# Kernel tuning notes

Measured on AMD Instinct MI355X. Metric: run time of the kernel, lower is better.

Reference implementation:

```python
import jax, jax.numpy as jnp
import numpy as np

B, N, D = 4096, 32768, 256


def setup_inputs() -> dict:
    key = jax.random.key(0)
    kx, kp = jax.random.split(key)
    x = jax.random.normal(kx, (B, D), dtype=jnp.float32)
    prototypes = jax.random.normal(kp, (N, D), dtype=jnp.float32)
    return {"x": x, "prototypes": prototypes}


def reference(x, prototypes):
    # Brute-force L2 1-NN: faiss IndexFlatL2 exact search, k=1, then gather
    x_sq = jnp.sum(x * x, axis=-1, keepdims=True)            # [B, 1]
    p_sq = jnp.sum(prototypes * prototypes, axis=-1)          # [N]
    dists = x_sq + p_sq[None, :] - 2.0 * (x @ prototypes.T)   # [B, N]
    idx = jnp.argmin(dists, axis=-1)                          # [B]
    return prototypes[idx]                                    # [B, D]
```

## Files before the change

### kernel.cpp

```cpp
#include <hip/hip_runtime.h>
#include <stdint.h>


#define NB 4096
#define NP 32768
#define ND 256
#define NG 512
#define MARGIN 2.0f
#define NSPLIT 8
#define CPB 4096

typedef __attribute__((ext_vector_type(8))) __bf16 bf16x8;
typedef __attribute__((ext_vector_type(4))) __bf16 bf16x4;
typedef __attribute__((ext_vector_type(4))) float f32x4;

static constexpr size_t OFF_PSQ = 0;
static constexpr size_t OFF_XB  = 131072;
static constexpr size_t OFF_PB  = OFF_XB + (size_t)NB * ND * 2;
static constexpr size_t OFF_BM  = OFF_PB + (size_t)NP * ND * 2;
static constexpr size_t WS_NEED = OFF_BM + (size_t)NB * NG * 4;

#define VMCNT(n) asm volatile("s_waitcnt vmcnt(" #n ")" ::: "memory")

__device__ __forceinline__ void gload_lds16(const void* g, void* l) {
    __builtin_amdgcn_global_load_lds(
        (const __attribute__((address_space(1))) uint32_t*)g,
        (__attribute__((address_space(3))) uint32_t*)l, 16, 0, 0);
}
__device__ __forceinline__ unsigned fkey(float f) {
    unsigned u = __float_as_uint(f);
    return (u & 0x80000000u) ? ~u : (u | 0x80000000u);
}
__device__ __forceinline__ float fkey_inv(unsigned u) {
    unsigned o = (u & 0x80000000u) ? (u & 0x7FFFFFFFu) : ~u;
    return __uint_as_float(o);
}
__device__ __forceinline__ unsigned long long umin64(unsigned long long a,
                                                     unsigned long long b) {
    return a < b ? a : b;
}
__device__ __forceinline__ unsigned umin32(unsigned a, unsigned b) {
    return a < b ? a : b;
}

__global__ void prep_kernel(const float* __restrict__ X, const float* __restrict__ P,
                            float* __restrict__ psq, __bf16* __restrict__ Xb,
                            __bf16* __restrict__ Pb) {
    int row  = blockIdx.x * 4 + (threadIdx.x >> 6);
    int lane = threadIdx.x & 63;
    if (row < NP) {
        f32x4 v = ((const f32x4*)(P + (size_t)row * ND))[lane];
        bf16x4 b;
        b.x = (__bf16)v.x; b.y = (__bf16)v.y; b.z = (__bf16)v.z; b.w = (__bf16)v.w;
        ((bf16x4*)(Pb + (size_t)row * ND))[lane] = b;
        float s = v.x*v.x + v.y*v.y + v.z*v.z + v.w*v.w;
        #pragma unroll
        for (int off = 32; off > 0; off >>= 1) s += __shfl_down(s, off);
        if (lane == 0) psq[row] = s;
    } else {
        int r = row - NP;
        f32x4 v = ((const f32x4*)(X + (size_t)r * ND))[lane];
        bf16x4 b;
        b.x = (__bf16)v.x; b.y = (__bf16)v.y; b.z = (__bf16)v.z; b.w = (__bf16)v.w;
        ((bf16x4*)(Xb + (size_t)r * ND))[lane] = b;
    }
}

__global__ __launch_bounds__(512, 2)
void nn_sweep8_kernel(const __bf16* __restrict__ Xb, const __bf16* __restrict__ Pb,
                      const float* __restrict__ psq,
                      unsigned* __restrict__ blockmin) {
    __shared__ __align__(16) char smem[114688];
    char*     ring    = smem;
    float*    psq_lds = (float*)(smem + 65536);
    unsigned* tbl     = (unsigned*)(smem + 81920);

    const int tid  = threadIdx.x;
    const int lane = tid & 63;
    const int wave = tid >> 6;
    const int wm = wave >> 2, wn = wave & 3;
    const int bid    = blockIdx.x;
    const int nsplit = bid & 7;
    const int mblk   = bid >> 3;
    const int bm     = mblk * 128;
    const int Nb     = nsplit * CPB;
    const int fr = lane & 15, kg = lane >> 4;
    const int wbase16 = (tid & ~63) * 16;

    bf16x8 a[4][8];
    #pragma unroll
    for (int mi = 0; mi < 4; ++mi)
        #pragma unroll
        for (int qq = 0; qq < 8; ++qq)
            a[mi][qq] = *(const bf16x8*)(Xb +
                (size_t)(bm + wm * 64 + mi * 16 + fr) * ND + qq * 32 + kg * 8);

    f32x4 acc[4][4];
    #pragma unroll
    for (int i = 0; i < 4; ++i)
        #pragma unroll
        for (int j = 0; j < 4; ++j) acc[i][j] = (f32x4){0.f, 0.f, 0.f, 0.f};

    auto stage = [&](int nn, int qq) {
        char* dst = ring + (size_t)(qq & 3) * 16384;
        const int colb = Nb + nn * 256;
        #pragma unroll
        for (int i = 0; i < 2; ++i) {
            const int c = i * 512 + tid;
            const int fn = c >> 6;
            const int l  = c & 63;
            gload_lds16(Pb + (size_t)(colb + fn * 16 + (l & 15)) * ND +
                            qq * 32 + (l >> 4) * 8,
                        dst + i * 8192 + wbase16);
        }
    };

    gload_lds16((const char*)(psq + Nb) + (size_t)tid * 16,
                (char*)psq_lds + wbase16);
    gload_lds16((const char*)(psq + Nb) + 8192 + (size_t)tid * 16,
                (char*)psq_lds + 8192 + wbase16);
    stage(0, 0); stage(0, 1); stage(0, 2);

    #pragma unroll 1
    for (int n = 0; n < 16; ++n) {
        #pragma unroll
        for (int q = 0; q < 8; ++q) {
            if (q == 6) { if (n == 15) { VMCNT(2); } else { VMCNT(4); } }
            else if (q == 7) { if (n == 15) { VMCNT(0); } else { VMCNT(4); } }
            else { VMCNT(4); }
            __builtin_amdgcn_s_barrier();
            __builtin_amdgcn_sched_barrier(0);

            if (q < 5) {
                stage(n, q + 3);
            } else if (n < 15) {
                stage(n + 1, q - 5);
            }

            const char* pc = ring + (size_t)(q & 3) * 16384;
            bf16x8 b[4];
            #pragma unroll
            for (int ni = 0; ni < 4; ++ni)
                b[ni] = *(const bf16x8*)(pc +
                         (size_t)((wn * 4 + ni) * 64 + lane) * 16);
            __builtin_amdgcn_s_setprio(1);
            #pragma unroll
            for (int mi = 0; mi < 4; ++mi)
                #pragma unroll
                for (int ni = 0; ni < 4; ++ni)
                    acc[mi][ni] = __builtin_amdgcn_mfma_f32_16x16x32_bf16(
                        a[mi][q], b[ni], acc[mi][ni], 0, 0, 0);
            __builtin_amdgcn_s_setprio(0);

            if (q == 7) {
                float cq[4];
                #pragma unroll
                for (int ni = 0; ni < 4; ++ni)
                    cq[ni] = psq_lds[n * 256 + wn * 64 + ni * 16 + fr];
                #pragma unroll
                for (int mi = 0; mi < 4; ++mi) {
                    #pragma unroll
                    for (int r = 0; r < 4; ++r) {
                        float d = fmaf(-2.f, acc[mi][0][r], cq[0]);
                        #pragma unroll
                        for (int ni = 1; ni < 4; ++ni)
                            d = fminf(d, fmaf(-2.f, acc[mi][ni][r], cq[ni]));
                        #pragma unroll
                        for (int m = 1; m < 16; m <<= 1)
                            d = fminf(d, __shfl_xor(d, m));
                        if (fr == 0)
                            tbl[(wm * 64 + mi * 16 + kg * 4 + r) * 64 +
                                (n * 4 + wn)] = fkey(d);
                    }
                }
                #pragma unroll
                for (int i = 0; i < 4; ++i)
                    #pragma unroll
                    for (int j = 0; j < 4; ++j)
                        acc[i][j] = (f32x4){0.f, 0.f, 0.f, 0.f};
            }
        }
    }

    __syncthreads();
    const int rl = tid >> 2;
    const int gb = (tid & 3) * 16;
    #pragma unroll
    for (int j = 0; j < 4; ++j) {
        *(uint4*)&blockmin[(size_t)(bm + rl) * NG + nsplit * 64 + gb + j * 4] =
            *(const uint4*)&tbl[rl * 64 + gb + j * 4];
    }
}

__global__ __launch_bounds__(256)
void rescore_kernel(const float* __restrict__ X, const float* __restrict__ P,
                    const float* __restrict__ psq,
                    const unsigned* __restrict__ blockmin,
                    float* __restrict__ out) {
    __shared__ float Xs[256];
    __shared__ float part[256];
    __shared__ unsigned keymin[256];
    __shared__ unsigned short cand[NG];
    __shared__ int cnt;
    __shared__ unsigned bcol_s;

    const int row = blockIdx.x;
    const int tid = threadIdx.x;
    const unsigned* bmr = blockmin + (size_t)row * NG;

    unsigned k0 = bmr[tid], k1 = bmr[tid + 256];
    if (tid < 64)
        ((f32x4*)Xs)[tid] = ((const f32x4*)(X + (size_t)row * ND))[tid];
    if (tid == 0) cnt = 0;
    keymin[tid] = umin32(k0, k1);
    __syncthreads();
    #pragma unroll
    for (int s = 128; s > 0; s >>= 1) {
        if (tid < s) keymin[tid] = umin32(keymin[tid], keymin[tid + s]);
        __syncthreads();
    }
    unsigned thr = fkey(fkey_inv(keymin[0]) + MARGIN);
    if (k0 <= thr) cand[atomicAdd(&cnt, 1)] = (unsigned short)tid;
    if (k1 <= thr) cand[atomicAdd(&cnt, 1)] = (unsigned short)(tid + 256);
    __syncthreads();

    const int n     = cnt;
    const int ct    = tid & 63;
    const int cpart = tid >> 6;
    unsigned long long best = 0xFFFFFFFFFFFFFFFFull;
    for (int c = 0; c < n; ++c) {
        int g = cand[c];
        int col = g * 64 + ct;
        const f32x4* p4 = (const f32x4*)(P + (size_t)col * ND + cpart * 64);
        const f32x4* x4 = (const f32x4*)(Xs + cpart * 64);
        float s = 0.f;
        #pragma unroll
        for (int i = 0; i < 16; ++i) {
            f32x4 pv = p4[i], xv = x4[i];
            s = fmaf(xv.x, pv.x, s); s = fmaf(xv.y, pv.y, s);
            s = fmaf(xv.z, pv.z, s); s = fmaf(xv.w, pv.w, s);
        }
        part[tid] = s;
        __syncthreads();
        if (tid < 64) {
            int col2 = g * 64 + tid;
            float tot = part[tid] + part[tid + 64] + part[tid + 128] + part[tid + 192];
            float d = fmaf(-2.f, tot, psq[col2]);
            best = umin64(best, ((unsigned long long)fkey(d) << 32) |
                                (unsigned long long)col2);
        }
        __syncthreads();
    }
    if (tid < 64) {
        #pragma unroll
        for (int m = 1; m < 64; m <<= 1)
            best = umin64(best, __shfl_xor(best, m));
        if (tid == 0) bcol_s = (unsigned)(best & 0xFFFFFFFFull);
    }
    __syncthreads();
    unsigned bc = bcol_s;
    if (tid < 64)
        ((f32x4*)(out + (size_t)row * ND))[tid] =
            ((const f32x4*)(P + (size_t)bc * ND))[tid];
}

#define BM1 128
#define BN1 128
#define BK1 32
#define LDA1 132

__global__ void psq_init_kernel(const float* __restrict__ P, float* __restrict__ psq,
                                unsigned long long* __restrict__ minpack) {
    int row  = blockIdx.x * 4 + (threadIdx.x >> 6);
    int lane = threadIdx.x & 63;
    float4 p4 = ((const float4*)(P + (size_t)row * ND))[lane];
    float s = p4.x*p4.x + p4.y*p4.y + p4.z*p4.z + p4.w*p4.w;
    #pragma unroll
    for (int off = 32; off > 0; off >>= 1) s += __shfl_down(s, off);
    if (lane == 0) psq[row] = s;
    int gid = blockIdx.x * blockDim.x + threadIdx.x;
    if (gid < NB) minpack[gid] = 0xFFFFFFFFFFFFFFFFull;
}

__global__ __launch_bounds__(256, 2)
void nn_main_kernel(const float* __restrict__ X, const float* __restrict__ P,
                    const float* __restrict__ psq,
                    unsigned long long* __restrict__ minpack) {
    __shared__ __align__(16) char smem_raw[2 * BK1 * LDA1 * 4];
    float (*As)[LDA1] = (float (*)[LDA1])smem_raw;
    float (*Bs)[LDA1] = (float (*)[LDA1])(smem_raw + BK1 * LDA1 * 4);
    const int bm  = blockIdx.y * BM1;
    const int bn  = blockIdx.x * BN1;
    const int tid = threadIdx.x;
    const int tx  = tid & 15;
    const int ty  = tid >> 4;
    float acc[8][8];
    #pragma unroll
    for (int i = 0; i < 8; ++i)
        #pragma unroll
        for (int j = 0; j < 8; ++j) acc[i][j] = 0.f;
    const int lrow = tid >> 3;
    const int lk   = (tid & 7) * 4;
    for (int k0 = 0; k0 < ND; k0 += BK1) {
        #pragma unroll
        for (int p = 0; p < 4; ++p) {
            int r = p * 32 + lrow;
            float4 a = *(const float4*)(X + (size_t)(bm + r) * ND + k0 + lk);
            As[lk+0][r] = a.x; As[lk+1][r] = a.y; As[lk+2][r] = a.z; As[lk+3][r] = a.w;
            float4 b = *(const float4*)(P + (size_t)(bn + r) * ND + k0 + lk);
            Bs[lk+0][r] = b.x; Bs[lk+1][r] = b.y; Bs[lk+2][r] = b.z; Bs[lk+3][r] = b.w;
        }
        __syncthreads();
        #pragma unroll 4
        for (int k = 0; k < BK1; ++k) {
            float4 a0 = *(const float4*)&As[k][ty*8];
            float4 a1 = *(const float4*)&As[k][ty*8 + 4];
            float4 b0 = *(const float4*)&Bs[k][tx*4];
            float4 b1 = *(const float4*)&Bs[k][64 + tx*4];
            float av[8] = {a0.x,a0.y,a0.z,a0.w,a1.x,a1.y,a1.z,a1.w};
            float bv[8] = {b0.x,b0.y,b0.z,b0.w,b1.x,b1.y,b1.z,b1.w};
            #pragma unroll
            for (int i = 0; i < 8; ++i)
                #pragma unroll
                for (int j = 0; j < 8; ++j)
                    acc[i][j] = fmaf(av[i], bv[j], acc[i][j]);
        }
        __syncthreads();
    }
    unsigned long long (*red)[16] = (unsigned long long (*)[16])smem_raw;
    float cj[8];
    int   jglob[8];
    #pragma unroll
    for (int j = 0; j < 8; ++j) {
        int c = (j < 4) ? (tx*4 + j) : (64 + tx*4 + (j - 4));
        jglob[j] = bn + c;
        cj[j]    = psq[bn + c];
    }
    #pragma unroll
    for (int i = 0; i < 8; ++i) {
        float best = 0.f; unsigned bidx = 0u; bool first = true;
        #pragma unroll
        for (int j = 0; j < 8; ++j) {
            float s = fmaf(-2.f, acc[i][j], cj[j]);
            if (first || s < best) { best = s; bidx = (unsigned)jglob[j]; first = false; }
        }
        unsigned u = fkey(best);
        red[ty*8 + i][tx] = ((unsigned long long)u << 32) | (unsigned long long)bidx;
    }
    __syncthreads();
    if (tid < BM1) {
        unsigned long long m = red[tid][0];
        #pragma unroll
        for (int t = 1; t < 16; ++t) m = umin64(m, red[tid][t]);
        atomicMin(&minpack[bm + tid], m);
    }
}

__global__ void gather_kernel(const float* __restrict__ P,
                              const unsigned long long* __restrict__ minpack,
                              float* __restrict__ out) {
    int row = blockIdx.x;
    unsigned idx = (unsigned)(minpack[row] & 0xFFFFFFFFull);
    int lane = threadIdx.x;
    ((float4*)(out + (size_t)row * ND))[lane] =
        ((const float4*)(P + (size_t)idx * ND))[lane];
}

extern "C" void kernel_launch(void* const* d_in, const int* in_sizes, int n_in,
                              void* d_out, int out_size, void* d_ws, size_t ws_size,
                              hipStream_t stream) {
    const float* X = (const float*)d_in[0];
    const float* P = (const float*)d_in[1];
    float* out = (float*)d_out;
    char* w = (char*)d_ws;

    if (ws_size >= WS_NEED) {
        float* psq = (float*)(w + OFF_PSQ);
        __bf16* Xb = (__bf16*)(w + OFF_XB);
        __bf16* Pb = (__bf16*)(w + OFF_PB);
        unsigned* blockmin = (unsigned*)(w + OFF_BM);

        prep_kernel<<<(NP + NB) / 4, 256, 0, stream>>>(X, P, psq, Xb, Pb);
        nn_sweep8_kernel<<<(NB / 128) * NSPLIT, 512, 0, stream>>>(Xb, Pb, psq,
                                                                  blockmin);
        rescore_kernel<<<NB, 256, 0, stream>>>(X, P, psq, blockmin, out);
    } else {
        float* psq = (float*)w;
        unsigned long long* minpack = (unsigned long long*)(w + (size_t)NP * 4);
        psq_init_kernel<<<NP / 4, 256, 0, stream>>>(P, psq, minpack);
        dim3 grid(NP / BN1, NB / BM1);
        nn_main_kernel<<<grid, dim3(256), 0, stream>>>(X, P, psq, minpack);
        gather_kernel<<<NB, 64, 0, stream>>>(P, minpack, out);
    }
}
```

Before: 193.5 us.

## Replace LDS-staged sweep with per-wave register-streamed prototype loads

```diff
diff --git a/kernel.cpp b/kernel.cpp
--- a/kernel.cpp
+++ b/kernel.cpp
@@ -7,8 +7,6 @@
 #define ND 256
 #define NG 512
 #define MARGIN 2.0f
-#define NSPLIT 8
-#define CPB 4096
 
 typedef __attribute__((ext_vector_type(8))) __bf16 bf16x8;
 typedef __attribute__((ext_vector_type(4))) __bf16 bf16x4;
@@ -20,13 +18,6 @@
 static constexpr size_t OFF_BM  = OFF_PB + (size_t)NP * ND * 2;
 static constexpr size_t WS_NEED = OFF_BM + (size_t)NB * NG * 4;
 
-#define VMCNT(n) asm volatile("s_waitcnt vmcnt(" #n ")" ::: "memory")
-
-__device__ __forceinline__ void gload_lds16(const void* g, void* l) {
-    __builtin_amdgcn_global_load_lds(
-        (const __attribute__((address_space(1))) uint32_t*)g,
-        (__attribute__((address_space(3))) uint32_t*)l, 16, 0, 0);
-}
 __device__ __forceinline__ unsigned fkey(float f) {
     unsigned u = __float_as_uint(f);
     return (u & 0x80000000u) ? ~u : (u | 0x80000000u);
@@ -66,34 +57,27 @@
     }
 }
 
-__global__ __launch_bounds__(512, 2)
-void nn_sweep8_kernel(const __bf16* __restrict__ Xb, const __bf16* __restrict__ Pb,
+__global__ __launch_bounds__(256, 2)
+void nn_stream_kernel(const __bf16* __restrict__ Xb, const __bf16* __restrict__ Pb,
                       const float* __restrict__ psq,
                       unsigned* __restrict__ blockmin) {
-    __shared__ __align__(16) char smem[114688];
-    char*     ring    = smem;
-    float*    psq_lds = (float*)(smem + 65536);
-    unsigned* tbl     = (unsigned*)(smem + 81920);
-
     const int tid  = threadIdx.x;
     const int lane = tid & 63;
     const int wave = tid >> 6;
-    const int wm = wave >> 2, wn = wave & 3;
     const int bid    = blockIdx.x;
-    const int nsplit = bid & 7;
-    const int mblk   = bid >> 3;
-    const int bm     = mblk * 128;
-    const int Nb     = nsplit * CPB;
+    const int rowblk = bid >> 5;
+    const int split  = bid & 31;
+    const int bm     = rowblk * 256 + wave * 64;
+    const int colb0  = split * 1024;
     const int fr = lane & 15, kg = lane >> 4;
-    const int wbase16 = (tid & ~63) * 16;
 
     bf16x8 a[4][8];
     #pragma unroll
     for (int mi = 0; mi < 4; ++mi)
         #pragma unroll
-        for (int qq = 0; qq < 8; ++qq)
-            a[mi][qq] = *(const bf16x8*)(Xb +
-                (size_t)(bm + wm * 64 + mi * 16 + fr) * ND + qq * 32 + kg * 8);
+        for (int kq = 0; kq < 8; ++kq)
+            a[mi][kq] = *(const bf16x8*)(Xb +
+                (size_t)(bm + mi * 16 + fr) * ND + kq * 32 + kg * 8);
 
     f32x4 acc[4][4];
     #pragma unroll
@@ -101,94 +85,65 @@
         #pragma unroll
         for (int j = 0; j < 4; ++j) acc[i][j] = (f32x4){0.f, 0.f, 0.f, 0.f};
 
-    auto stage = [&](int nn, int qq) {
-        char* dst = ring + (size_t)(qq & 3) * 16384;
-        const int colb = Nb + nn * 256;
-        #pragma unroll
-        for (int i = 0; i < 2; ++i) {
-            const int c = i * 512 + tid;
-            const int fn = c >> 6;
-            const int l  = c & 63;
-            gload_lds16(Pb + (size_t)(colb + fn * 16 + (l & 15)) * ND +
-                            qq * 32 + (l >> 4) * 8,
-                        dst + i * 8192 + wbase16);
-        }
-    };
-
-    gload_lds16((const char*)(psq + Nb) + (size_t)tid * 16,
-                (char*)psq_lds + wbase16);
-    gload_lds16((const char*)(psq + Nb) + 8192 + (size_t)tid * 16,
-                (char*)psq_lds + 8192 + wbase16);
-    stage(0, 0); stage(0, 1); stage(0, 2);
+    const __bf16* pbase = Pb + (size_t)(colb0 + fr) * ND + kg * 8;
+
+    bf16x8 bv[2][4];
+    #pragma unroll
+    for (int ni = 0; ni < 4; ++ni)
+        bv[0][ni] = *(const bf16x8*)(pbase + (size_t)(ni * 16) * ND);
 
     #pragma unroll 1
-    for (int n = 0; n < 16; ++n) {
-        #pragma unroll
-        for (int q = 0; q < 8; ++q) {
-            if (q == 6) { if (n == 15) { VMCNT(2); } else { VMCNT(4); } }
-            else if (q == 7) { if (n == 15) { VMCNT(0); } else { VMCNT(4); } }
-            else { VMCNT(4); }
-            __builtin_amdgcn_s_barrier();
-            __builtin_amdgcn_sched_barrier(0);
-
-            if (q < 5) {
-                stage(n, q + 3);
-            } else if (n < 15) {
-                stage(n + 1, q - 5);
+    for (int t = 0; t < 16; ++t) {
+        float cq[4];
+        #pragma unroll
+        for (int ni = 0; ni < 4; ++ni)
+            cq[ni] = psq[colb0 + t * 64 + ni * 16 + fr];
+
+        #pragma unroll
+        for (int kq = 0; kq < 8; ++kq) {
+            const int cur = kq & 1, nxt = cur ^ 1;
+            if (kq < 7) {
+                #pragma unroll
+                for (int ni = 0; ni < 4; ++ni)
+                    bv[nxt][ni] = *(const bf16x8*)(pbase +
+                        (size_t)(t * 64 + ni * 16) * ND + (kq + 1) * 32);
+            } else {
+                const int t2 = (t + 1) & 15;
+                #pragma unroll
+                for (int ni = 0; ni < 4; ++ni)
+                    bv[nxt][ni] = *(const bf16x8*)(pbase +
+                        (size_t)(t2 * 64 + ni * 16) * ND);
             }
-
-            const char* pc = ring + (size_t)(q & 3) * 16384;
-            bf16x8 b[4];
-            #pragma unroll
-            for (int ni = 0; ni < 4; ++ni)
-                b[ni] = *(const bf16x8*)(pc +
-                         (size_t)((wn * 4 + ni) * 64 + lane) * 16);
-            __builtin_amdgcn_s_setprio(1);
             #pragma unroll
             for (int mi = 0; mi < 4; ++mi)
                 #pragma unroll
                 for (int ni = 0; ni < 4; ++ni)
                     acc[mi][ni] = __builtin_amdgcn_mfma_f32_16x16x32_bf16(
-                        a[mi][q], b[ni], acc[mi][ni], 0, 0, 0);
-            __builtin_amdgcn_s_setprio(0);
-
-            if (q == 7) {
-                float cq[4];
-                #pragma unroll
-                for (int ni = 0; ni < 4; ++ni)
-                    cq[ni] = psq_lds[n * 256 + wn * 64 + ni * 16 + fr];
-                #pragma unroll
-                for (int mi = 0; mi < 4; ++mi) {
-                    #pragma unroll
-                    for (int r = 0; r < 4; ++r) {
-                        float d = fmaf(-2.f, acc[mi][0][r], cq[0]);
-                        #pragma unroll
-                        for (int ni = 1; ni < 4; ++ni)
-                            d = fminf(d, fmaf(-2.f, acc[mi][ni][r], cq[ni]));
-                        #pragma unroll
-                        for (int m = 1; m < 16; m <<= 1)
-                            d = fminf(d, __shfl_xor(d, m));
-                        if (fr == 0)
-                            tbl[(wm * 64 + mi * 16 + kg * 4 + r) * 64 +
-                                (n * 4 + wn)] = fkey(d);
-                    }
-                }
-                #pragma unroll
-                for (int i = 0; i < 4; ++i)
-                    #pragma unroll
-                    for (int j = 0; j < 4; ++j)
-                        acc[i][j] = (f32x4){0.f, 0.f, 0.f, 0.f};
+                        a[mi][kq], bv[cur][ni], acc[mi][ni], 0, 0, 0);
+        }
+
+        const int g = split * 16 + t;
+        #pragma unroll
+        for (int mi = 0; mi < 4; ++mi) {
+            #pragma unroll
+            for (int r = 0; r < 4; ++r) {
+                float d = fmaf(-2.f, acc[mi][0][r], cq[0]);
+                #pragma unroll
+                for (int ni = 1; ni < 4; ++ni)
+                    d = fminf(d, fmaf(-2.f, acc[mi][ni][r], cq[ni]));
+                #pragma unroll
+                for (int m = 1; m < 16; m <<= 1)
+                    d = fminf(d, __shfl_xor(d, m));
+                if (fr == 0)
+                    blockmin[(size_t)(bm + mi * 16 + kg * 4 + r) * NG + g] =
+                        fkey(d);
             }
         }
-    }
-
-    __syncthreads();
-    const int rl = tid >> 2;
-    const int gb = (tid & 3) * 16;
-    #pragma unroll
-    for (int j = 0; j < 4; ++j) {
-        *(uint4*)&blockmin[(size_t)(bm + rl) * NG + nsplit * 64 + gb + j * 4] =
-            *(const uint4*)&tbl[rl * 64 + gb + j * 4];
+        #pragma unroll
+        for (int i = 0; i < 4; ++i)
+            #pragma unroll
+            for (int j = 0; j < 4; ++j)
+                acc[i][j] = (f32x4){0.f, 0.f, 0.f, 0.f};
     }
 }
 
@@ -381,8 +336,7 @@
         unsigned* blockmin = (unsigned*)(w + OFF_BM);
 
         prep_kernel<<<(NP + NB) / 4, 256, 0, stream>>>(X, P, psq, Xb, Pb);
-        nn_sweep8_kernel<<<(NB / 128) * NSPLIT, 512, 0, stream>>>(Xb, Pb, psq,
-                                                                  blockmin);
+        nn_stream_kernel<<<512, 256, 0, stream>>>(Xb, Pb, psq, blockmin);
         rescore_kernel<<<NB, 256, 0, stream>>>(X, P, psq, blockmin, out);
     } else {
         float* psq = (float*)w;
```

Result: slower. 227.1 us (+17.4%).

## Deepen LDS ring to six stages with register double-buffered B, wave-per-row rescore

Applied to the files above, without the earlier changes.

```diff
diff --git a/kernel.cpp b/kernel.cpp
--- a/kernel.cpp
+++ b/kernel.cpp
@@ -21,6 +21,7 @@
 static constexpr size_t WS_NEED = OFF_BM + (size_t)NB * NG * 4;
 
 #define VMCNT(n) asm volatile("s_waitcnt vmcnt(" #n ")" ::: "memory")
+#define LGKM0()  asm volatile("s_waitcnt lgkmcnt(0)" ::: "memory")
 
 __device__ __forceinline__ void gload_lds16(const void* g, void* l) {
     __builtin_amdgcn_global_load_lds(
@@ -67,13 +68,13 @@
 }
 
 __global__ __launch_bounds__(512, 2)
-void nn_sweep8_kernel(const __bf16* __restrict__ Xb, const __bf16* __restrict__ Pb,
-                      const float* __restrict__ psq,
-                      unsigned* __restrict__ blockmin) {
-    __shared__ __align__(16) char smem[114688];
+void nn_pipe_kernel(const __bf16* __restrict__ Xb, const __bf16* __restrict__ Pb,
+                    const float* __restrict__ psq,
+                    unsigned* __restrict__ blockmin) {
+    __shared__ __align__(16) char smem[147456];
     char*     ring    = smem;
-    float*    psq_lds = (float*)(smem + 65536);
-    unsigned* tbl     = (unsigned*)(smem + 81920);
+    float*    psq_lds = (float*)(smem + 98304);
+    unsigned* tbl     = (unsigned*)(smem + 114688);
 
     const int tid  = threadIdx.x;
     const int lane = tid & 63;
@@ -101,85 +102,117 @@
         #pragma unroll
         for (int j = 0; j < 4; ++j) acc[i][j] = (f32x4){0.f, 0.f, 0.f, 0.f};
 
-    auto stage = [&](int nn, int qq) {
-        char* dst = ring + (size_t)(qq & 3) * 16384;
-        const int colb = Nb + nn * 256;
+    auto stage = [&](int p) {
+        char* dst = ring + (size_t)(p % 6) * 16384;
+        const int colb = Nb + (p >> 3) * 256;
+        const int kq   = p & 7;
         #pragma unroll
         for (int i = 0; i < 2; ++i) {
             const int c = i * 512 + tid;
             const int fn = c >> 6;
             const int l  = c & 63;
             gload_lds16(Pb + (size_t)(colb + fn * 16 + (l & 15)) * ND +
-                            qq * 32 + (l >> 4) * 8,
+                            kq * 32 + (l >> 4) * 8,
                         dst + i * 8192 + wbase16);
         }
     };
+
+    bf16x8 bv[2][4];
 
     gload_lds16((const char*)(psq + Nb) + (size_t)tid * 16,
                 (char*)psq_lds + wbase16);
     gload_lds16((const char*)(psq + Nb) + 8192 + (size_t)tid * 16,
                 (char*)psq_lds + 8192 + wbase16);
-    stage(0, 0); stage(0, 1); stage(0, 2);
+    stage(0); stage(1); stage(2); stage(3); stage(4);
+    VMCNT(8);
+    __builtin_amdgcn_s_barrier();
+    __builtin_amdgcn_sched_barrier(0);
+    #pragma unroll
+    for (int ni = 0; ni < 4; ++ni)
+        bv[0][ni] = *(const bf16x8*)(ring +
+                     (size_t)((wn * 4 + ni) * 64 + lane) * 16);
+
+    auto epi = [&](int nt) {
+        float cq[4];
+        #pragma unroll
+        for (int ni = 0; ni < 4; ++ni)
+            cq[ni] = psq_lds[nt * 256 + wn * 64 + ni * 16 + fr];
+        #pragma unroll
+        for (int mi = 0; mi < 4; ++mi) {
+            #pragma unroll
+            for (int r = 0; r < 4; ++r) {
+                float d = fmaf(-2.f, acc[mi][0][r], cq[0]);
+                #pragma unroll
+                for (int ni = 1; ni < 4; ++ni)
+                    d = fminf(d, fmaf(-2.f, acc[mi][ni][r], cq[ni]));
+                #pragma unroll
+                for (int m = 1; m < 16; m <<= 1)
+                    d = fminf(d, __shfl_xor(d, m));
+                if (fr == 0)
+                    tbl[(wm * 64 + mi * 16 + kg * 4 + r) * 64 + (nt * 4 + wn)] =
+                        fkey(d);
+            }
+        }
+        #pragma unroll
+        for (int i = 0; i < 4; ++i)
+            #pragma unroll
+            for (int j = 0; j < 4; ++j)
+                acc[i][j] = (f32x4){0.f, 0.f, 0.f, 0.f};
+    };
 
     #pragma unroll 1
-    for (int n = 0; n < 16; ++n) {
+    for (int nt = 0; nt < 15; ++nt) {
         #pragma unroll
         for (int q = 0; q < 8; ++q) {
-            if (q == 6) { if (n == 15) { VMCNT(2); } else { VMCNT(4); } }
-            else if (q == 7) { if (n == 15) { VMCNT(0); } else { VMCNT(4); } }
-            else { VMCNT(4); }
+            const int cur = q & 1, nxt = cur ^ 1;
+            const int t = nt * 8 + q;
+            VMCNT(6);
             __builtin_amdgcn_s_barrier();
             __builtin_amdgcn_sched_barrier(0);
-
-            if (q < 5) {
-                stage(n, q + 3);
-            } else if (n < 15) {
-                stage(n + 1, q - 5);
-            }
-
-            const char* pc = ring + (size_t)(q & 3) * 16384;
-            bf16x8 b[4];
+            const char* pc = ring + (size_t)(((t + 1) % 6)) * 16384;
             #pragma unroll
             for (int ni = 0; ni < 4; ++ni)
-                b[ni] = *(const bf16x8*)(pc +
-                         (size_t)((wn * 4 + ni) * 64 + lane) * 16);
+                bv[nxt][ni] = *(const bf16x8*)(pc +
+                    (size_t)((wn * 4 + ni) * 64 + lane) * 16);
+            stage(t + 5);
             __builtin_amdgcn_s_setprio(1);
             #pragma unroll
             for (int mi = 0; mi < 4; ++mi)
                 #pragma unroll
                 for (int ni = 0; ni < 4; ++ni)
                     acc[mi][ni] = __builtin_amdgcn_mfma_f32_16x16x32_bf16(
-                        a[mi][q], b[ni], acc[mi][ni], 0, 0, 0);
+                        a[mi][q], bv[cur][ni], acc[mi][ni], 0, 0, 0);
             __builtin_amdgcn_s_setprio(0);
-
-            if (q == 7) {
-                float cq[4];
-                #pragma unroll
-                for (int ni = 0; ni < 4; ++ni)
-                    cq[ni] = psq_lds[n * 256 + wn * 64 + ni * 16 + fr];
-                #pragma unroll
-                for (int mi = 0; mi < 4; ++mi) {
-                    #pragma unroll
-                    for (int r = 0; r < 4; ++r) {
-                        float d = fmaf(-2.f, acc[mi][0][r], cq[0]);
-                        #pragma unroll
-                        for (int ni = 1; ni < 4; ++ni)
-                            d = fminf(d, fmaf(-2.f, acc[mi][ni][r], cq[ni]));
-                        #pragma unroll
-                        for (int m = 1; m < 16; m <<= 1)
-                            d = fminf(d, __shfl_xor(d, m));
-                        if (fr == 0)
-                            tbl[(wm * 64 + mi * 16 + kg * 4 + r) * 64 +
-                                (n * 4 + wn)] = fkey(d);
-                    }
-                }
-                #pragma unroll
-                for (int i = 0; i < 4; ++i)
-                    #pragma unroll
-                    for (int j = 0; j < 4; ++j)
-                        acc[i][j] = (f32x4){0.f, 0.f, 0.f, 0.f};
-            }
-        }
+            if (q == 7) epi(nt);
+        }
+    }
+    #pragma unroll
+    for (int q = 0; q < 8; ++q) {
+        const int cur = q & 1, nxt = cur ^ 1;
+        const int t = 120 + q;
+        if (q <= 3)      { VMCNT(6); }
+        else if (q == 4) { VMCNT(4); }
+        else if (q == 5) { VMCNT(2); }
+        else if (q == 6) { VMCNT(0); }
+        if (q < 7) {
+            __builtin_amdgcn_s_barrier();
+            __builtin_amdgcn_sched_barrier(0);
+            const char* pc = ring + (size_t)(((t + 1) % 6)) * 16384;
+            #pragma unroll
+            for (int ni = 0; ni < 4; ++ni)
+                bv[nxt][ni] = *(const bf16x8*)(pc +
+                    (size_t)((wn * 4 + ni) * 64 + lane) * 16);
+            if (q < 3) stage(t + 5);
+        }
+        __builtin_amdgcn_s_setprio(1);
+        #pragma unroll
+        for (int mi = 0; mi < 4; ++mi)
+            #pragma unroll
+            for (int ni = 0; ni < 4; ++ni)
+                acc[mi][ni] = __builtin_amdgcn_mfma_f32_16x16x32_bf16(
+                    a[mi][q], bv[cur][ni], acc[mi][ni], 0, 0, 0);
+        __builtin_amdgcn_s_setprio(0);
+        if (q == 7) epi(15);
     }
 
     __syncthreads();
@@ -192,76 +225,60 @@
     }
 }
 
-__global__ __launch_bounds__(256)
-void rescore_kernel(const float* __restrict__ X, const float* __restrict__ P,
-                    const float* __restrict__ psq,
-                    const unsigned* __restrict__ blockmin,
-                    float* __restrict__ out) {
-    __shared__ float Xs[256];
-    __shared__ float part[256];
-    __shared__ unsigned keymin[256];
-    __shared__ unsigned short cand[NG];
-    __shared__ int cnt;
-    __shared__ unsigned bcol_s;
-
-    const int row = blockIdx.x;
-    const int tid = threadIdx.x;
+__global__ __launch_bounds__(512, 2)
+void rescore_wave_kernel(const float* __restrict__ X, const float* __restrict__ P,
+                         const float* __restrict__ psq,
+                         const unsigned* __restrict__ blockmin,
+                         float* __restrict__ out) {
+    __shared__ float Xs[8][256];
+    __shared__ unsigned short wcand[8][512];
+    __shared__ int wcnt[8];
+
+    const int tid = threadIdx.x, lane = tid & 63, wv = tid >> 6;
+    const int row = blockIdx.x * 8 + wv;
+
+    ((f32x4*)Xs[wv])[lane] = ((const f32x4*)(X + (size_t)row * ND))[lane];
+    if (lane == 0) wcnt[wv] = 0;
+
     const unsigned* bmr = blockmin + (size_t)row * NG;
-
-    unsigned k0 = bmr[tid], k1 = bmr[tid + 256];
-    if (tid < 64)
-        ((f32x4*)Xs)[tid] = ((const f32x4*)(X + (size_t)row * ND))[tid];
-    if (tid == 0) cnt = 0;
-    keymin[tid] = umin32(k0, k1);
-    __syncthreads();
-    #pragma unroll
-    for (int s = 128; s > 0; s >>= 1) {
-        if (tid < s) keymin[tid] = umin32(keymin[tid], keymin[tid + s]);
-        __syncthreads();
-    }
-    unsigned thr = fkey(fkey_inv(keymin[0]) + MARGIN);
-    if (k0 <= thr) cand[atomicAdd(&cnt, 1)] = (unsigned short)tid;
-    if (k1 <= thr) cand[atomicAdd(&cnt, 1)] = (unsigned short)(tid + 256);
-    __syncthreads();
-
-    const int n     = cnt;
-    const int ct    = tid & 63;
-    const int cpart = tid >> 6;
+    uint4 ka = ((const uint4*)bmr)[lane * 2];
+    uint4 kb = ((const uint4*)bmr)[lane * 2 + 1];
+    unsigned km = umin32(umin32(umin32(ka.x, ka.y), umin32(ka.z, ka.w)),
+                         umin32(umin32(kb.x, kb.y), umin32(kb.z, kb.w)));
+    #pragma unroll
+    for (int m = 1; m < 64; m <<= 1) km = umin32(km, __shfl_xor(km, m));
+    const unsigned thr = fkey(fkey_inv(km) + MARGIN);
+
+    const unsigned k8[8] = {ka.x, ka.y, ka.z, ka.w, kb.x, kb.y, kb.z, kb.w};
+    #pragma unroll
+    for (int i = 0; i < 8; ++i)
+        if (k8[i] <= thr)
+            wcand[wv][atomicAdd(&wcnt[wv], 1)] = (unsigned short)(lane * 8 + i);
+    LGKM0();
+    const int n = wcnt[wv];
+
     unsigned long long best = 0xFFFFFFFFFFFFFFFFull;
+    const f32x4* x4 = (const f32x4*)Xs[wv];
     for (int c = 0; c < n; ++c) {
-        int g = cand[c];
-        int col = g * 64 + ct;
-        const f32x4* p4 = (const f32x4*)(P + (size_t)col * ND + cpart * 64);
-        const f32x4* x4 = (const f32x4*)(Xs + cpart * 64);
+        const int col = (int)wcand[wv][c] * 64 + lane;
+        const f32x4* p4 = (const f32x4*)(P + (size_t)col * ND);
         float s = 0.f;
-        #pragma unroll
-        for (int i = 0; i < 16; ++i) {
+        #pragma unroll 16
+        for (int i = 0; i < 64; ++i) {
             f32x4 pv = p4[i], xv = x4[i];
             s = fmaf(xv.x, pv.x, s); s = fmaf(xv.y, pv.y, s);
             s = fmaf(xv.z, pv.z, s); s = fmaf(xv.w, pv.w, s);
         }
-        part[tid] = s;
-        __syncthreads();
-        if (tid < 64) {
-            int col2 = g * 64 + tid;
-            float tot = part[tid] + part[tid + 64] + part[tid + 128] + part[tid + 192];
-            float d = fmaf(-2.f, tot, psq[col2]);
-            best = umin64(best, ((unsigned long long)fkey(d) << 32) |
-                                (unsigned long long)col2);
-        }
-        __syncthreads();
-    }
-    if (tid < 64) {
-        #pragma unroll
-        for (int m = 1; m < 64; m <<= 1)
-            best = umin64(best, __shfl_xor(best, m));
-        if (tid == 0) bcol_s = (unsigned)(best & 0xFFFFFFFFull);
-    }
-    __syncthreads();
-    unsigned bc = bcol_s;
-    if (tid < 64)
-        ((f32x4*)(out + (size_t)row * ND))[tid] =
-            ((const f32x4*)(P + (size_t)bc * ND))[tid];
+        float d = fmaf(-2.f, s, psq[col]);
+        best = umin64(best, ((unsigned long long)fkey(d) << 32) |
+                            (unsigned long long)(unsigned)col);
+    }
+    #pragma unroll
+    for (int m = 1; m < 64; m <<= 1)
+        best = umin64(best, __shfl_xor(best, m));
+    const unsigned bc = (unsigned)(best & 0xFFFFFFFFull);
+    ((f32x4*)(out + (size_t)row * ND))[lane] =
+        ((const f32x4*)(P + (size_t)bc * ND))[lane];
 }
 
 #define BM1 128
@@ -305,10 +322,10 @@
         #pragma unroll
         for (int p = 0; p < 4; ++p) {
             int r = p * 32 + lrow;
-            float4 a = *(const float4*)(X + (size_t)(bm + r) * ND + k0 + lk);
-            As[lk+0][r] = a.x; As[lk+1][r] = a.y; As[lk+2][r] = a.z; As[lk+3][r] = a.w;
-            float4 b = *(const float4*)(P + (size_t)(bn + r) * ND + k0 + lk);
-            Bs[lk+0][r] = b.x; Bs[lk+1][r] = b.y; Bs[lk+2][r] = b.z; Bs[lk+3][r] = b.w;
+            float4 aa = *(const float4*)(X + (size_t)(bm + r) * ND + k0 + lk);
+            As[lk+0][r] = aa.x; As[lk+1][r] = aa.y; As[lk+2][r] = aa.z; As[lk+3][r] = aa.w;
+            float4 bb = *(const float4*)(P + (size_t)(bn + r) * ND + k0 + lk);
+            Bs[lk+0][r] = bb.x; Bs[lk+1][r] = bb.y; Bs[lk+2][r] = bb.z; Bs[lk+3][r] = bb.w;
         }
         __syncthreads();
         #pragma unroll 4
@@ -318,12 +335,12 @@
             float4 b0 = *(const float4*)&Bs[k][tx*4];
             float4 b1 = *(const float4*)&Bs[k][64 + tx*4];
             float av[8] = {a0.x,a0.y,a0.z,a0.w,a1.x,a1.y,a1.z,a1.w};
-            float bv[8] = {b0.x,b0.y,b0.z,b0.w,b1.x,b1.y,b1.z,b1.w};
+            float bvv[8] = {b0.x,b0.y,b0.z,b0.w,b1.x,b1.y,b1.z,b1.w};
             #pragma unroll
             for (int i = 0; i < 8; ++i)
                 #pragma unroll
                 for (int j = 0; j < 8; ++j)
-                    acc[i][j] = fmaf(av[i], bv[j], acc[i][j]);
+                    acc[i][j] = fmaf(av[i], bvv[j], acc[i][j]);
         }
         __syncthreads();
     }
@@ -338,13 +355,13 @@
     }
     #pragma unroll
     for (int i = 0; i < 8; ++i) {
-        float best = 0.f; unsigned bidx = 0u; bool first = true;
+        float bestv = 0.f; unsigned bidx = 0u; bool first = true;
         #pragma unroll
         for (int j = 0; j < 8; ++j) {
             float s = fmaf(-2.f, acc[i][j], cj[j]);
-            if (first || s < best) { best = s; bidx = (unsigned)jglob[j]; first = false; }
-        }
-        unsigned u = fkey(best);
+            if (first || s < bestv) { bestv = s; bidx = (unsigned)jglob[j]; first = false; }
+        }
+        unsigned u = fkey(bestv);
         red[ty*8 + i][tx] = ((unsigned long long)u << 32) | (unsigned long long)bidx;
     }
     __syncthreads();
@@ -381,9 +398,9 @@
         unsigned* blockmin = (unsigned*)(w + OFF_BM);
 
         prep_kernel<<<(NP + NB) / 4, 256, 0, stream>>>(X, P, psq, Xb, Pb);
-        nn_sweep8_kernel<<<(NB / 128) * NSPLIT, 512, 0, stream>>>(Xb, Pb, psq,
-                                                                  blockmin);
-        rescore_kernel<<<NB, 256, 0, stream>>>(X, P, psq, blockmin, out);
+        nn_pipe_kernel<<<(NB / 128) * NSPLIT, 512, 0, stream>>>(Xb, Pb, psq,
+                                                                blockmin);
+        rescore_wave_kernel<<<NB / 8, 512, 0, stream>>>(X, P, psq, blockmin, out);
     } else {
         float* psq = (float*)w;
         unsigned long long* minpack = (unsigned long long*)(w + (size_t)NP * 4);
```

After: 226.9 us. 1.17x slower.
